# Kernel tuning notes

Hardware: AMD Instinct MI355X
Metric: run time of the kernel (lower is better)

The kernel has to match this reference:

```python
import jax, jax.numpy as jnp
import numpy as np

BETA = 0.25
NUM_CODES = 1024
EMBED_DIM = 256


def setup_inputs() -> dict:
    key = jax.random.key(0)
    k1, k2 = jax.random.split(key)
    z = jax.random.normal(k1, (64, 32, 32, EMBED_DIM), dtype=jnp.float32)
    # torch init: uniform(-1/num_codes, 1/num_codes)
    codebook = jax.random.uniform(k2, (NUM_CODES, EMBED_DIM), dtype=jnp.float32,
                                  minval=-1.0 / NUM_CODES, maxval=1.0 / NUM_CODES)
    return {"z": z, "codebook": codebook}


def reference(z, codebook):
    shape = z.shape
    z_flat = z.reshape(-1, EMBED_DIM)  # [N, D]
    # squared-distance matrix: ||z||^2 + ||c||^2 - 2 z c^T  -> [N, K]
    d = (jnp.sum(z_flat * z_flat, axis=1, keepdims=True)
         + jnp.sum(codebook * codebook, axis=1)
         - 2.0 * jnp.einsum('nd,kd->nk', z_flat, codebook))
    codes = jnp.argmin(d, axis=1)              # [N] int
    quantized = codebook[codes]                # [N, D] gather
    sg = jax.lax.stop_gradient
    cb_loss = jnp.mean((quantized - sg(z_flat)) ** 2)
    cmt_loss = jnp.mean((z_flat - sg(quantized)) ** 2)
    vq_loss = cb_loss + BETA * cmt_loss
    # straight-through estimator
    out = z_flat + sg(quantized - z_flat)
    return out.reshape(shape), codes.reshape(shape[:-1]), vq_loss
```

## Files before the change

### kernel.cpp

```cpp
#include <hip/hip_runtime.h>


#define N_PTS    65536
#define K_CODES  1024
#define DIM      256
#define MARGIN   1.5e-4f
#define WSKIP    4096

#define OUT_VALS  16777216
#define OUT_CODES 65536

typedef __attribute__((ext_vector_type(8))) short short8v;
typedef __attribute__((ext_vector_type(8))) _Float16 half8v;
typedef __attribute__((ext_vector_type(4))) float float4v;

__device__ __forceinline__ int perm_idx(int r, int k) {
  return ((((r >> 4) * 8 + (k >> 5)) * 4 + ((k >> 3) & 3)) * 128) + (r & 15) * 8 + (k & 7);
}

__device__ __forceinline__ short f2h_bits(float x) {
  union { _Float16 h; short s; } u;
  u.h = (_Float16)x;
  return u.s;
}

__device__ __forceinline__ void gload16(const void* g, void* l) {
  __builtin_amdgcn_global_load_lds(
      (const __attribute__((address_space(1))) unsigned*)g,
      (__attribute__((address_space(3))) unsigned*)l, 16, 0, 0);
}

__global__ void prep_cb_kernel(const float* __restrict__ cb,
                               short* __restrict__ cbh_perm,
                               float* __restrict__ Bf,
                               unsigned long long* __restrict__ scratch,
                               unsigned long long* __restrict__ ws0) {
  const int gid = blockIdx.x * 256 + threadIdx.x;
  scratch[gid] = ~0ull;
  if (gid < 512) ws0[gid] = 0ull;
  int r    = blockIdx.x * 4 + (threadIdx.x >> 6);
  int lane = threadIdx.x & 63;
  const float4 v = *(const float4*)(cb + (size_t)r * DIM + lane * 4);
  double s = (double)v.x * v.x + (double)v.y * v.y
           + (double)v.z * v.z + (double)v.w * v.w;
#pragma unroll
  for (int off = 32; off > 0; off >>= 1) s += __shfl_down(s, off);
  if (lane == 0) Bf[r] = (float)s;
  short4 h = make_short4(f2h_bits(v.x * 1024.0f), f2h_bits(v.y * 1024.0f),
                         f2h_bits(v.z * 1024.0f), f2h_bits(v.w * 1024.0f));
  *(short4*)(cbh_perm + perm_idx(r, lane * 4)) = h;
}

__global__ __launch_bounds__(256, 4) void argmin_mfma_kernel(
    const float* __restrict__ z, const float* __restrict__ cb,
    const short* __restrict__ cbh_perm,
    const float* __restrict__ Bf, float* __restrict__ outq,
    float* __restrict__ codes_out,
    int* __restrict__ cnt2, int* __restrict__ cntf,
    unsigned* __restrict__ flag2, int* __restrict__ flagf,
    float* __restrict__ bv2a, float* __restrict__ bvfa,
    double* __restrict__ loss_slots) {
  __shared__ __align__(16) short lbuf[2][8192];
  __shared__ double wls[4];
  const int t    = threadIdx.x;
  const int w    = t >> 6;
  const int l    = t & 63;
  const int quad = l >> 4;
  const int lr   = l & 15;
  const int m0   = blockIdx.x * 64;

  {
    const char* src = (const char*)cbh_perm;
    char* dst = (char*)&lbuf[0][0];
#pragma unroll
    for (int i = 0; i < 4; ++i)
      gload16(src + t * 16 + i * 4096, dst + t * 16 + i * 4096);
  }

  half8v ah[8];
  {
    const float* zrow = z + (size_t)(m0 + w * 16 + lr) * DIM;
#pragma unroll
    for (int q = 0; q < 8; ++q) {
      float4 p0 = *(const float4*)(zrow + q * 32 + quad * 8);
      float4 p1 = *(const float4*)(zrow + q * 32 + quad * 8 + 4);
      half8v h;
      h[0] = (_Float16)p0.x; h[1] = (_Float16)p0.y;
      h[2] = (_Float16)p0.z; h[3] = (_Float16)p0.w;
      h[4] = (_Float16)p1.x; h[5] = (_Float16)p1.y;
      h[6] = (_Float16)p1.z; h[7] = (_Float16)p1.w;
      ah[q] = h;
    }
  }

  float bestv[4], secv[4], thirdv[4]; int bestk[4], seck[4];
#pragma unroll
  for (int r = 0; r < 4; ++r) {
    bestv[r] = 3.0e38f; secv[r] = 3.0e38f; thirdv[r] = 3.0e38f;
    bestk[r] = 0; seck[r] = 0;
  }

  __syncthreads();
  int cur = 0;
  for (int it = 0; it < 32; ++it) {
    if (it < 31) {
      const char* src = (const char*)cbh_perm + (size_t)(it + 1) * 16384;
      char* dst = (char*)&lbuf[cur ^ 1][0];
#pragma unroll
      for (int i = 0; i < 4; ++i)
        gload16(src + t * 16 + i * 4096, dst + t * 16 + i * 4096);
    }
    const int c0 = it * 32;
#pragma unroll
    for (int st = 0; st < 2; ++st) {
      float4v acc = {0.f, 0.f, 0.f, 0.f};
#pragma unroll
      for (int q = 0; q < 8; ++q) {
        half8v b = *(const half8v*)(&lbuf[cur][(st * 8 + q) * 512 + quad * 128 + lr * 8]);
        acc = __builtin_amdgcn_mfma_f32_16x16x32_f16(ah[q], b, acc, 0, 0, 0);
      }
      const int k = c0 + st * 16 + lr;
      const float bkf = Bf[k];
#pragma unroll
      for (int r = 0; r < 4; ++r) {
        float v = fmaf(-0.001953125f, acc[r], bkf);
        bool lt1 = v < bestv[r];
        bool lt2 = v < secv[r];
        thirdv[r] = fminf(fmaxf(v, secv[r]), thirdv[r]);
        secv[r]   = fminf(fmaxf(v, bestv[r]), secv[r]);
        bestv[r]  = fminf(v, bestv[r]);
        seck[r]   = lt1 ? bestk[r] : (lt2 ? k : seck[r]);
        bestk[r]  = lt1 ? k : bestk[r];
      }
    }
    __syncthreads();
    cur ^= 1;
  }

#pragma unroll
  for (int mask = 1; mask < 16; mask <<= 1) {
#pragma unroll
    for (int r = 0; r < 4; ++r) {
      float ov  = __shfl_xor(bestv[r], mask);
      float os  = __shfl_xor(secv[r], mask);
      float ot  = __shfl_xor(thirdv[r], mask);
      int   ok  = __shfl_xor(bestk[r], mask);
      int   osk = __shfl_xor(seck[r], mask);
      bool win = (ov < bestv[r]) || (ov == bestv[r] && ok < bestk[r]);
      float a1 = win ? ov : bestv[r], a2 = win ? os : secv[r], a3 = win ? ot : thirdv[r];
      int   a1k = win ? ok : bestk[r], a2k = win ? osk : seck[r];
      float b1 = win ? bestv[r] : ov, b2 = win ? secv[r] : os;
      int   b1k = win ? bestk[r] : ok;
      bool s2 = (a2 < b1) || (a2 == b1 && a2k < b1k);
      bestv[r] = a1; bestk[r] = a1k;
      secv[r] = s2 ? a2 : b1; seck[r] = s2 ? a2k : b1k;
      thirdv[r] = s2 ? fminf(a3, b1) : fminf(a2, b2);
    }
  }

  if (m0 >= WSKIP) {
#pragma unroll
    for (int p = 0; p < 16; ++p) {
      int c = __shfl(bestk[p & 3], (p >> 2) << 4);
      int n = m0 + w * 16 + p;
      *(float4*)(outq + (size_t)n * DIM + l * 4) =
          *(const float4*)(cb + (size_t)c * DIM + l * 4);
    }
  }

  double ls = 0.0;
  if (lr == 0)
    ls = (double)bestv[0] + (double)bestv[1] + (double)bestv[2] + (double)bestv[3];
  ls += __shfl_down(ls, 16);
  ls += __shfl_down(ls, 32);
  if (l == 0) wls[w] = ls;

  if (lr == 0) {
#pragma unroll
    for (int r = 0; r < 4; ++r) {
      int n = m0 + w * 16 + quad * 4 + r;
      codes_out[n] = (float)bestk[r];
      if (thirdv[r] - bestv[r] < MARGIN) {
        int pos = atomicAdd(cntf, 1);
        flagf[pos] = n; bvfa[pos] = bestv[r];
      } else if (secv[r] - bestv[r] < MARGIN) {
        int pos = atomicAdd(cnt2, 1);
        flag2[pos] = (unsigned)n | ((unsigned)seck[r] << 16);
        bv2a[pos] = bestv[r];
      }
    }
  }
  __syncthreads();
  if (t == 0)
    atomicAdd(&loss_slots[blockIdx.x & 255], wls[0] + wls[1] + wls[2] + wls[3]);
}

__global__ __launch_bounds__(256) void fixup_pair_kernel(
    const float* __restrict__ z, const float* __restrict__ cb,
    const float* __restrict__ Bf, const unsigned* __restrict__ flag2,
    const int* __restrict__ cnt2, const float* __restrict__ bv2a,
    float* __restrict__ codes_out, float* __restrict__ outq,
    double* __restrict__ loss_slots) {
  const int t   = threadIdx.x;
  const int l   = t & 63;
  const int h   = l >> 5;
  const int sub = l & 31;
  const int wid = blockIdx.x * 4 + (t >> 6);
  const int nw  = gridDim.x * 4;
  const int cnt = *cnt2;
  for (int i = wid; i < cnt; i += nw) {
    const unsigned rec = flag2[i];
    const int n  = rec & 0xFFFF;
    const int k2 = rec >> 16;
    const int k1 = (int)codes_out[n];
    const int k  = h ? k2 : k1;
    const float* zr = z + (size_t)n * DIM + sub * 8;
    const float* cr = cb + (size_t)k * DIM + sub * 8;
    const float4 za = *(const float4*)(zr);
    const float4 zb = *(const float4*)(zr + 4);
    const float4 ca = *(const float4*)(cr);
    const float4 cv = *(const float4*)(cr + 4);
    double s = (double)za.x*za.x + (double)za.y*za.y + (double)za.z*za.z + (double)za.w*za.w
             + (double)zb.x*zb.x + (double)zb.y*zb.y + (double)zb.z*zb.z + (double)zb.w*zb.w;
    double d = (double)za.x*ca.x + (double)za.y*ca.y + (double)za.z*ca.z + (double)za.w*ca.w
             + (double)zb.x*cv.x + (double)zb.y*cv.y + (double)zb.z*cv.z + (double)zb.w*cv.w;
#pragma unroll
    for (int m = 1; m < 32; m <<= 1) {
      s += __shfl_xor(s, m);
      d += __shfl_xor(d, m);
    }
    const float Sfl = (float)s;
    const float T1  = Sfl + Bf[k];
    const float v   = T1 - 2.0f * (float)d;
    const float vo  = __shfl_xor(v, 32);
    const int   ko  = __shfl_xor(k, 32);
    const bool keep = (v < vo) || (v == vo && k < ko);
    const float vmin = keep ? v : vo;
    const int   kf   = keep ? k : ko;
    if (l == 0) {
      codes_out[n] = (float)kf;
      atomicAdd(&loss_slots[n & 255], (double)(vmin - bv2a[i]));
    }
    if (kf != k1 && n >= WSKIP)
      *(float4*)(outq + (size_t)n * DIM + l * 4) =
          *(const float4*)(cb + (size_t)kf * DIM + l * 4);
  }
}

__global__ __launch_bounds__(256) void fixup_full_kernel(
    const float* __restrict__ z, const float* __restrict__ cb,
    const float* __restrict__ Bf, const int* __restrict__ flagf,
    const int* __restrict__ cntf, unsigned long long* __restrict__ scratch) {
  __shared__ float vred[4];
  __shared__ int   kred[4];
  const int t = threadIdx.x;
  const int w = t >> 6;
  const int l = t & 63;
  const int cnt = *cntf;
  for (int ib = blockIdx.x; (ib >> 2) < cnt; ib += gridDim.x) {
    const int i = ib >> 2, q = ib & 3;
    const int n = flagf[i];
    const float4 zv = *(const float4*)(z + (size_t)n * DIM + l * 4);
    double s = (double)zv.x*zv.x + (double)zv.y*zv.y
             + (double)zv.z*zv.z + (double)zv.w*zv.w;
#pragma unroll
    for (int off = 32; off > 0; off >>= 1) s += __shfl_xor(s, off);
    const float Sfl = (float)s;
    float bvv = 3.0e38f; int bkk = 0;
    const int kbase = q * 256 + w * 64;
#pragma unroll 4
    for (int k0 = 0; k0 < 64; ++k0) {
      const int k = kbase + k0;
      const float4 cv = *(const float4*)(cb + (size_t)k * DIM + l * 4);
      double d = (double)zv.x*cv.x + (double)zv.y*cv.y
               + (double)zv.z*cv.z + (double)zv.w*cv.w;
#pragma unroll
      for (int off = 32; off > 0; off >>= 1) d += __shfl_xor(d, off);
      float T1 = Sfl + Bf[k];
      float v  = T1 - 2.0f * (float)d;
      if (v < bvv) { bvv = v; bkk = k; }
    }
    __syncthreads();
    if (l == 0) { vred[w] = bvv; kred[w] = bkk; }
    __syncthreads();
    if (t == 0) {
      float fv = vred[0]; int fk = kred[0];
#pragma unroll
      for (int j = 1; j < 4; ++j) {
        float v2 = vred[j]; int kk = kred[j];
        if (v2 < fv || (v2 == fv && kk < fk)) { fv = v2; fk = kk; }
      }
      unsigned long long key =
          ((unsigned long long)__float_as_uint(fv) << 32) | (unsigned)fk;
      atomicMin(&scratch[n], key);
    }
  }
}

__global__ __launch_bounds__(256) void fixup_write_kernel(
    const int* __restrict__ flagf, const int* __restrict__ cntf,
    const unsigned long long* __restrict__ scratch,
    const float* __restrict__ bvfa, const float* __restrict__ cb,
    float* __restrict__ codes_out, float* __restrict__ outq,
    double* __restrict__ loss_slots) {
  const int t = threadIdx.x, l = t & 63;
  const int wid = blockIdx.x * 4 + (t >> 6);
  const int nw  = gridDim.x * 4;
  const int cnt = *cntf;
  for (int i = wid; i < cnt; i += nw) {
    const int n = flagf[i];
    const unsigned long long key = scratch[n];
    const int   fk = (int)(unsigned)(key & 0xFFFFFFFFull);
    const float fv = __uint_as_float((unsigned)(key >> 32));
    const int   k1 = (int)codes_out[n];
    if (l == 0) {
      codes_out[n] = (float)fk;
      atomicAdd(&loss_slots[n & 255], (double)(fv - bvfa[i]));
    }
    if (fk != k1 && n >= WSKIP)
      *(float4*)(outq + (size_t)n * DIM + l * 4) =
          *(const float4*)(cb + (size_t)fk * DIM + l * 4);
  }
}

__global__ void small_gather_kernel(const float* __restrict__ cb,
                                    const float* __restrict__ codes_f,
                                    float* __restrict__ outq) {
  int gid = blockIdx.x * 256 + threadIdx.x;
  int n = gid >> 6, l = gid & 63;
  int c = (int)codes_f[n];
  *(float4*)(outq + (size_t)n * DIM + l * 4) =
      *(const float4*)(cb + (size_t)c * DIM + l * 4);
}

__global__ void finalize_kernel(const double* __restrict__ loss_slots,
                                float* __restrict__ out_loss) {
  const int t = threadIdx.x;
  double s = loss_slots[t];
#pragma unroll
  for (int off = 32; off > 0; off >>= 1) s += __shfl_down(s, off);
  __shared__ double ws[4];
  if ((t & 63) == 0) ws[t >> 6] = s;
  __syncthreads();
  if (t == 0) {
    double tot = ws[0] + ws[1] + ws[2] + ws[3];
    out_loss[0] = (float)(1.25 * tot / (double)(N_PTS * (size_t)DIM));
  }
}

extern "C" void kernel_launch(void* const* d_in, const int* in_sizes, int n_in,
                              void* d_out, int out_size, void* d_ws, size_t ws_size,
                              hipStream_t stream) {
  const float* z  = (const float*)d_in[0];
  const float* cb = (const float*)d_in[1];
  float* out = (float*)d_out;
  double* loss_slots = (double*)d_ws;
  int*      cnt2  = (int*)((char*)d_ws + 2048);
  int*      cntf  = (int*)((char*)d_ws + 2052);
  float*    Bf    = (float*)((char*)d_ws + 4096);
  unsigned* flag2 = (unsigned*)((char*)d_ws + 8192);
  short* cbh_perm = (short*)d_out;
  float* bv2a     = (float*)((char*)d_out + 524288);
  float* bvfa     = (float*)((char*)d_out + 786432);
  unsigned long long* scratch = (unsigned long long*)((char*)d_out + 1048576);
  int*   flagf    = (int*)((char*)d_out + 1572864);

  prep_cb_kernel<<<K_CODES / 4, 256, 0, stream>>>(
      cb, cbh_perm, Bf, scratch, (unsigned long long*)d_ws);
  argmin_mfma_kernel<<<N_PTS / 64, 256, 0, stream>>>(
      z, cb, cbh_perm, Bf, out, out + OUT_VALS, cnt2, cntf, flag2, flagf,
      bv2a, bvfa, loss_slots);
  fixup_pair_kernel<<<1024, 256, 0, stream>>>(
      z, cb, Bf, flag2, cnt2, bv2a, out + OUT_VALS, out, loss_slots);
  fixup_full_kernel<<<2048, 256, 0, stream>>>(z, cb, Bf, flagf, cntf, scratch);
  fixup_write_kernel<<<64, 256, 0, stream>>>(
      flagf, cntf, scratch, bvfa, cb, out + OUT_VALS, out, loss_slots);
  small_gather_kernel<<<WSKIP * 64 / 256, 256, 0, stream>>>(
      cb, out + OUT_VALS, out);
  finalize_kernel<<<1, 256, 0, stream>>>(loss_slots, out + OUT_VALS + OUT_CODES);
}
```

Before: 201.1 us.

## Split codebook across wave halves and reuse B fragments over two row tiles

Blocks grow to 512 threads covering 128 points. Each wave pair splits the codebook in half, and each wave computes two 16-row tiles against every B fragment it loads, so one LDS read feeds two MFMAs. The two halves' top-3 candidates are merged through shared memory. The kernel now also computes the full squared distance including ||z||² for the loss and flagging, and the quantized gather reads codes from shared memory. The cost is more registers per thread, which may lower occupancy.

Result: slower. 226.1 us (+12.4%).

```diff
diff --git a/kernel.cpp b/kernel.cpp
--- a/kernel.cpp
+++ b/kernel.cpp
@@ -51,7 +51,7 @@
   *(short4*)(cbh_perm + perm_idx(r, lane * 4)) = h;
 }
 
-__global__ __launch_bounds__(256, 4) void argmin_mfma_kernel(
+__global__ __launch_bounds__(512, 4) void argmin_mfma_kernel(
     const float* __restrict__ z, const float* __restrict__ cb,
     const short* __restrict__ cbh_perm,
     const float* __restrict__ Bf, float* __restrict__ outq,
@@ -60,77 +60,98 @@
     unsigned* __restrict__ flag2, int* __restrict__ flagf,
     float* __restrict__ bv2a, float* __restrict__ bvfa,
     double* __restrict__ loss_slots) {
-  __shared__ __align__(16) short lbuf[2][8192];
-  __shared__ double wls[4];
+  __shared__ __align__(16) short lbuf[2][2][4096];
+  __shared__ float mv1[128][2], mv2[128][2], mv3[128][2];
+  __shared__ int   mk1[128][2], mk2[128][2];
+  __shared__ float mz[128];
+  __shared__ int   scodes[128];
+  __shared__ double wls[2];
   const int t    = threadIdx.x;
   const int w    = t >> 6;
   const int l    = t & 63;
   const int quad = l >> 4;
   const int lr   = l & 15;
-  const int m0   = blockIdx.x * 64;
+  const int wp   = w >> 1;
+  const int h    = w & 1;
+  const int m0   = blockIdx.x * 128;
+  const int pbase = m0 + wp * 32;
 
   {
-    const char* src = (const char*)cbh_perm;
-    char* dst = (char*)&lbuf[0][0];
-#pragma unroll
-    for (int i = 0; i < 4; ++i)
-      gload16(src + t * 16 + i * 4096, dst + t * 16 + i * 4096);
-  }
-
-  half8v ah[8];
-  {
-    const float* zrow = z + (size_t)(m0 + w * 16 + lr) * DIM;
+    const char* src = (const char*)cbh_perm + (size_t)(h * 32) * 8192 + wp * 2048;
+    char* dst = (char*)&lbuf[h][0][0] + wp * 2048;
+    gload16(src + l * 16, dst + l * 16);
+    gload16(src + 1024 + l * 16, dst + 1024 + l * 16);
+  }
+
+  half8v ah[2][8];
+  float Szrow[2];
+#pragma unroll
+  for (int a = 0; a < 2; ++a) {
+    const float* zrow = z + (size_t)(pbase + a * 16 + lr) * DIM;
+    double zs = 0.0;
 #pragma unroll
     for (int q = 0; q < 8; ++q) {
       float4 p0 = *(const float4*)(zrow + q * 32 + quad * 8);
       float4 p1 = *(const float4*)(zrow + q * 32 + quad * 8 + 4);
-      half8v h;
-      h[0] = (_Float16)p0.x; h[1] = (_Float16)p0.y;
-      h[2] = (_Float16)p0.z; h[3] = (_Float16)p0.w;
-      h[4] = (_Float16)p1.x; h[5] = (_Float16)p1.y;
-      h[6] = (_Float16)p1.z; h[7] = (_Float16)p1.w;
-      ah[q] = h;
-    }
-  }
-
-  float bestv[4], secv[4], thirdv[4]; int bestk[4], seck[4];
-#pragma unroll
-  for (int r = 0; r < 4; ++r) {
-    bestv[r] = 3.0e38f; secv[r] = 3.0e38f; thirdv[r] = 3.0e38f;
-    bestk[r] = 0; seck[r] = 0;
+      zs = fma((double)p0.x, (double)p0.x, zs);
+      zs = fma((double)p0.y, (double)p0.y, zs);
+      zs = fma((double)p0.z, (double)p0.z, zs);
+      zs = fma((double)p0.w, (double)p0.w, zs);
+      zs = fma((double)p1.x, (double)p1.x, zs);
+      zs = fma((double)p1.y, (double)p1.y, zs);
+      zs = fma((double)p1.z, (double)p1.z, zs);
+      zs = fma((double)p1.w, (double)p1.w, zs);
+      half8v hh;
+      hh[0] = (_Float16)p0.x; hh[1] = (_Float16)p0.y;
+      hh[2] = (_Float16)p0.z; hh[3] = (_Float16)p0.w;
+      hh[4] = (_Float16)p1.x; hh[5] = (_Float16)p1.y;
+      hh[6] = (_Float16)p1.z; hh[7] = (_Float16)p1.w;
+      ah[a][q] = hh;
+    }
+    zs += __shfl_xor(zs, 16);
+    zs += __shfl_xor(zs, 32);
+    Szrow[a] = (float)zs;
+  }
+
+  float bv[8], sv[8], tv[8]; int bk[8], sk[8];
+#pragma unroll
+  for (int s = 0; s < 8; ++s) {
+    bv[s] = 3.0e38f; sv[s] = 3.0e38f; tv[s] = 3.0e38f; bk[s] = 0; sk[s] = 0;
   }
 
   __syncthreads();
   int cur = 0;
   for (int it = 0; it < 32; ++it) {
     if (it < 31) {
-      const char* src = (const char*)cbh_perm + (size_t)(it + 1) * 16384;
-      char* dst = (char*)&lbuf[cur ^ 1][0];
-#pragma unroll
-      for (int i = 0; i < 4; ++i)
-        gload16(src + t * 16 + i * 4096, dst + t * 16 + i * 4096);
-    }
-    const int c0 = it * 32;
-#pragma unroll
-    for (int st = 0; st < 2; ++st) {
-      float4v acc = {0.f, 0.f, 0.f, 0.f};
-#pragma unroll
-      for (int q = 0; q < 8; ++q) {
-        half8v b = *(const half8v*)(&lbuf[cur][(st * 8 + q) * 512 + quad * 128 + lr * 8]);
-        acc = __builtin_amdgcn_mfma_f32_16x16x32_f16(ah[q], b, acc, 0, 0, 0);
-      }
-      const int k = c0 + st * 16 + lr;
-      const float bkf = Bf[k];
+      const char* src = (const char*)cbh_perm + (size_t)(h * 32 + it + 1) * 8192 + wp * 2048;
+      char* dst = (char*)&lbuf[h][cur ^ 1][0] + wp * 2048;
+      gload16(src + l * 16, dst + l * 16);
+      gload16(src + 1024 + l * 16, dst + 1024 + l * 16);
+    }
+    const short* bb = &lbuf[h][cur][0];
+    float4v acc0 = {0.f, 0.f, 0.f, 0.f};
+    float4v acc1 = {0.f, 0.f, 0.f, 0.f};
+#pragma unroll
+    for (int q = 0; q < 8; ++q) {
+      half8v b = *(const half8v*)(bb + q * 512 + quad * 128 + lr * 8);
+      acc0 = __builtin_amdgcn_mfma_f32_16x16x32_f16(ah[0][q], b, acc0, 0, 0, 0);
+      acc1 = __builtin_amdgcn_mfma_f32_16x16x32_f16(ah[1][q], b, acc1, 0, 0, 0);
+    }
+    const int k = (h * 32 + it) * 16 + lr;
+    const float bkf = Bf[k];
+#pragma unroll
+    for (int a = 0; a < 2; ++a) {
 #pragma unroll
       for (int r = 0; r < 4; ++r) {
-        float v = fmaf(-0.001953125f, acc[r], bkf);
-        bool lt1 = v < bestv[r];
-        bool lt2 = v < secv[r];
-        thirdv[r] = fminf(fmaxf(v, secv[r]), thirdv[r]);
-        secv[r]   = fminf(fmaxf(v, bestv[r]), secv[r]);
-        bestv[r]  = fminf(v, bestv[r]);
-        seck[r]   = lt1 ? bestk[r] : (lt2 ? k : seck[r]);
-        bestk[r]  = lt1 ? k : bestk[r];
+        const int s = a * 4 + r;
+        float v = fmaf(-0.001953125f, a ? acc1[r] : acc0[r], bkf);
+        bool lt1 = v < bv[s];
+        bool lt2 = v < sv[s];
+        tv[s] = fminf(fmaxf(v, sv[s]), tv[s]);
+        sv[s] = fminf(fmaxf(v, bv[s]), sv[s]);
+        bv[s] = fminf(v, bv[s]);
+        sk[s] = lt1 ? bk[s] : (lt2 ? k : sk[s]);
+        bk[s] = lt1 ? k : bk[s];
       }
     }
     __syncthreads();
@@ -140,59 +161,86 @@
 #pragma unroll
   for (int mask = 1; mask < 16; mask <<= 1) {
 #pragma unroll
-    for (int r = 0; r < 4; ++r) {
-      float ov  = __shfl_xor(bestv[r], mask);
-      float os  = __shfl_xor(secv[r], mask);
-      float ot  = __shfl_xor(thirdv[r], mask);
-      int   ok  = __shfl_xor(bestk[r], mask);
-      int   osk = __shfl_xor(seck[r], mask);
-      bool win = (ov < bestv[r]) || (ov == bestv[r] && ok < bestk[r]);
-      float a1 = win ? ov : bestv[r], a2 = win ? os : secv[r], a3 = win ? ot : thirdv[r];
-      int   a1k = win ? ok : bestk[r], a2k = win ? osk : seck[r];
-      float b1 = win ? bestv[r] : ov, b2 = win ? secv[r] : os;
-      int   b1k = win ? bestk[r] : ok;
+    for (int s = 0; s < 8; ++s) {
+      float ov  = __shfl_xor(bv[s], mask);
+      float os  = __shfl_xor(sv[s], mask);
+      float ot  = __shfl_xor(tv[s], mask);
+      int   ok  = __shfl_xor(bk[s], mask);
+      int   osk = __shfl_xor(sk[s], mask);
+      bool win = (ov < bv[s]) || (ov == bv[s] && ok < bk[s]);
+      float a1 = win ? ov : bv[s], a2 = win ? os : sv[s], a3 = win ? ot : tv[s];
+      int   a1k = win ? ok : bk[s], a2k = win ? osk : sk[s];
+      float b1 = win ? bv[s] : ov, b2 = win ? sv[s] : os;
+      int   b1k = win ? bk[s] : ok;
       bool s2 = (a2 < b1) || (a2 == b1 && a2k < b1k);
-      bestv[r] = a1; bestk[r] = a1k;
-      secv[r] = s2 ? a2 : b1; seck[r] = s2 ? a2k : b1k;
-      thirdv[r] = s2 ? fminf(a3, b1) : fminf(a2, b2);
-    }
-  }
+      bv[s] = a1; bk[s] = a1k;
+      sv[s] = s2 ? a2 : b1; sk[s] = s2 ? a2k : b1k;
+      tv[s] = s2 ? fminf(a3, b1) : fminf(a2, b2);
+    }
+  }
+
+  if (lr == 0) {
+#pragma unroll
+    for (int a = 0; a < 2; ++a)
+#pragma unroll
+      for (int r = 0; r < 4; ++r) {
+        int s  = a * 4 + r;
+        int pt = wp * 32 + a * 16 + quad * 4 + r;
+        mv1[pt][h] = bv[s]; mv2[pt][h] = sv[s]; mv3[pt][h] = tv[s];
+        mk1[pt][h] = bk[s]; mk2[pt][h] = sk[s];
+      }
+  }
+  if (h == 0 && quad == 0) {
+#pragma unroll
+    for (int a = 0; a < 2; ++a)
+      mz[wp * 32 + a * 16 + lr] = Szrow[a];
+  }
+  __syncthreads();
+
+  double ls = 0.0;
+  if (t < 128) {
+    float a1 = mv1[t][0], a2 = mv2[t][0], a3 = mv3[t][0];
+    int   a1k = mk1[t][0], a2k = mk2[t][0];
+    float c1 = mv1[t][1], c2 = mv2[t][1], c3 = mv3[t][1];
+    int   c1k = mk1[t][1], c2k = mk2[t][1];
+    bool win = (c1 < a1) || (c1 == a1 && c1k < a1k);
+    float x1 = win ? c1 : a1, x2 = win ? c2 : a2, x3 = win ? c3 : a3;
+    int   x1k = win ? c1k : a1k, x2k = win ? c2k : a2k;
+    float y1 = win ? a1 : c1, y2 = win ? a2 : c2;
+    int   y1k = win ? a1k : c1k;
+    bool s2 = (x2 < y1) || (x2 == y1 && x2k < y1k);
+    float f2v = s2 ? x2 : y1; int f2k = s2 ? x2k : y1k;
+    float f3v = s2 ? fminf(x3, y1) : fminf(x2, y2);
+    int n = m0 + t;
+    codes_out[n] = (float)x1k;
+    scodes[t] = x1k;
+    float vrow = mz[t] + x1;
+    ls = (double)vrow;
+    if (f3v - x1 < MARGIN) {
+      int pos = atomicAdd(cntf, 1);
+      flagf[pos] = n; bvfa[pos] = vrow;
+    } else if (f2v - x1 < MARGIN) {
+      int pos = atomicAdd(cnt2, 1);
+      flag2[pos] = (unsigned)n | ((unsigned)f2k << 16);
+      bv2a[pos] = vrow;
+    }
+  }
+#pragma unroll
+  for (int off = 32; off > 0; off >>= 1) ls += __shfl_down(ls, off);
+  if (l == 0 && w < 2) wls[w] = ls;
+  __syncthreads();
 
   if (m0 >= WSKIP) {
 #pragma unroll
-    for (int p = 0; p < 16; ++p) {
-      int c = __shfl(bestk[p & 3], (p >> 2) << 4);
-      int n = m0 + w * 16 + p;
-      *(float4*)(outq + (size_t)n * DIM + l * 4) =
+    for (int i = 0; i < 16; ++i) {
+      int row = i * 8 + w;
+      int c = scodes[row];
+      *(float4*)(outq + (size_t)(m0 + row) * DIM + l * 4) =
           *(const float4*)(cb + (size_t)c * DIM + l * 4);
     }
   }
-
-  double ls = 0.0;
-  if (lr == 0)
-    ls = (double)bestv[0] + (double)bestv[1] + (double)bestv[2] + (double)bestv[3];
-  ls += __shfl_down(ls, 16);
-  ls += __shfl_down(ls, 32);
-  if (l == 0) wls[w] = ls;
-
-  if (lr == 0) {
-#pragma unroll
-    for (int r = 0; r < 4; ++r) {
-      int n = m0 + w * 16 + quad * 4 + r;
-      codes_out[n] = (float)bestk[r];
-      if (thirdv[r] - bestv[r] < MARGIN) {
-        int pos = atomicAdd(cntf, 1);
-        flagf[pos] = n; bvfa[pos] = bestv[r];
-      } else if (secv[r] - bestv[r] < MARGIN) {
-        int pos = atomicAdd(cnt2, 1);
-        flag2[pos] = (unsigned)n | ((unsigned)seck[r] << 16);
-        bv2a[pos] = bestv[r];
-      }
-    }
-  }
-  __syncthreads();
   if (t == 0)
-    atomicAdd(&loss_slots[blockIdx.x & 255], wls[0] + wls[1] + wls[2] + wls[3]);
+    atomicAdd(&loss_slots[blockIdx.x & 255], wls[0] + wls[1]);
 }
 
 __global__ __launch_bounds__(256) void fixup_pair_kernel(
@@ -367,7 +415,7 @@
 
   prep_cb_kernel<<<K_CODES / 4, 256, 0, stream>>>(
       cb, cbh_perm, Bf, scratch, (unsigned long long*)d_ws);
-  argmin_mfma_kernel<<<N_PTS / 64, 256, 0, stream>>>(
+  argmin_mfma_kernel<<<N_PTS / 128, 512, 0, stream>>>(
       z, cb, cbh_perm, Bf, out, out + OUT_VALS, cnt2, cntf, flag2, flagf,
       bv2a, bvfa, loss_slots);
   fixup_pair_kernel<<<1024, 256, 0, stream>>>(
```

## Compute row norms in-kernel for loss and fuse finalize into gather kernel

Applied to the files above, without the earlier changes.

The argmin kernel now computes each z row's squared norm in double precision from the values it already loads, and adds it to the best partial distance. This gives the true squared error for the loss and for the fixup baselines, where before only the partial score was used. The final loss reduction is merged into the small gather kernel as one extra block, which saves one kernel launch. The fused block reads loss_slots in the same kernel that gathers rows, which is safe only because the fixup kernels run earlier on the stream. The double-precision FMAs add ALU work to the main kernel.

New measurement: 200.2 us. About the same (-0.5%).

```diff
diff --git a/kernel.cpp b/kernel.cpp
--- a/kernel.cpp
+++ b/kernel.cpp
@@ -78,12 +78,22 @@
   }
 
   half8v ah[8];
+  float Szrow;
   {
     const float* zrow = z + (size_t)(m0 + w * 16 + lr) * DIM;
+    double zs0 = 0.0, zs1 = 0.0;
 #pragma unroll
     for (int q = 0; q < 8; ++q) {
       float4 p0 = *(const float4*)(zrow + q * 32 + quad * 8);
       float4 p1 = *(const float4*)(zrow + q * 32 + quad * 8 + 4);
+      zs0 = fma((double)p0.x, (double)p0.x, zs0);
+      zs0 = fma((double)p0.y, (double)p0.y, zs0);
+      zs0 = fma((double)p0.z, (double)p0.z, zs0);
+      zs0 = fma((double)p0.w, (double)p0.w, zs0);
+      zs1 = fma((double)p1.x, (double)p1.x, zs1);
+      zs1 = fma((double)p1.y, (double)p1.y, zs1);
+      zs1 = fma((double)p1.z, (double)p1.z, zs1);
+      zs1 = fma((double)p1.w, (double)p1.w, zs1);
       half8v h;
       h[0] = (_Float16)p0.x; h[1] = (_Float16)p0.y;
       h[2] = (_Float16)p0.z; h[3] = (_Float16)p0.w;
@@ -91,6 +101,10 @@
       h[6] = (_Float16)p1.z; h[7] = (_Float16)p1.w;
       ah[q] = h;
     }
+    double zs = zs0 + zs1;
+    zs += __shfl_xor(zs, 16);
+    zs += __shfl_xor(zs, 32);
+    Szrow = (float)zs;
   }
 
   float bestv[4], secv[4], thirdv[4]; int bestk[4], seck[4];
@@ -158,6 +172,11 @@
     }
   }
 
+  float vrow[4];
+#pragma unroll
+  for (int r = 0; r < 4; ++r)
+    vrow[r] = __shfl(Szrow, quad * 4 + r) + bestv[r];
+
   if (m0 >= WSKIP) {
 #pragma unroll
     for (int p = 0; p < 16; ++p) {
@@ -170,7 +189,7 @@
 
   double ls = 0.0;
   if (lr == 0)
-    ls = (double)bestv[0] + (double)bestv[1] + (double)bestv[2] + (double)bestv[3];
+    ls = (double)vrow[0] + (double)vrow[1] + (double)vrow[2] + (double)vrow[3];
   ls += __shfl_down(ls, 16);
   ls += __shfl_down(ls, 32);
   if (l == 0) wls[w] = ls;
@@ -182,11 +201,11 @@
       codes_out[n] = (float)bestk[r];
       if (thirdv[r] - bestv[r] < MARGIN) {
         int pos = atomicAdd(cntf, 1);
-        flagf[pos] = n; bvfa[pos] = bestv[r];
+        flagf[pos] = n; bvfa[pos] = vrow[r];
       } else if (secv[r] - bestv[r] < MARGIN) {
         int pos = atomicAdd(cnt2, 1);
         flag2[pos] = (unsigned)n | ((unsigned)seck[r] << 16);
-        bv2a[pos] = bestv[r];
+        bv2a[pos] = vrow[r];
       }
     }
   }
@@ -323,29 +342,30 @@
   }
 }
 
-__global__ void small_gather_kernel(const float* __restrict__ cb,
-                                    const float* __restrict__ codes_f,
-                                    float* __restrict__ outq) {
+__global__ void gather_finalize_kernel(const float* __restrict__ cb,
+                                       const float* __restrict__ codes_f,
+                                       float* __restrict__ outq,
+                                       const double* __restrict__ loss_slots,
+                                       float* __restrict__ out_loss) {
+  if (blockIdx.x == WSKIP / 4) {
+    const int t = threadIdx.x;
+    double s = loss_slots[t];
+#pragma unroll
+    for (int off = 32; off > 0; off >>= 1) s += __shfl_down(s, off);
+    __shared__ double ws[4];
+    if ((t & 63) == 0) ws[t >> 6] = s;
+    __syncthreads();
+    if (t == 0) {
+      double tot = ws[0] + ws[1] + ws[2] + ws[3];
+      out_loss[0] = (float)(1.25 * tot / (double)(N_PTS * (size_t)DIM));
+    }
+    return;
+  }
   int gid = blockIdx.x * 256 + threadIdx.x;
   int n = gid >> 6, l = gid & 63;
   int c = (int)codes_f[n];
   *(float4*)(outq + (size_t)n * DIM + l * 4) =
       *(const float4*)(cb + (size_t)c * DIM + l * 4);
-}
-
-__global__ void finalize_kernel(const double* __restrict__ loss_slots,
-                                float* __restrict__ out_loss) {
-  const int t = threadIdx.x;
-  double s = loss_slots[t];
-#pragma unroll
-  for (int off = 32; off > 0; off >>= 1) s += __shfl_down(s, off);
-  __shared__ double ws[4];
-  if ((t & 63) == 0) ws[t >> 6] = s;
-  __syncthreads();
-  if (t == 0) {
-    double tot = ws[0] + ws[1] + ws[2] + ws[3];
-    out_loss[0] = (float)(1.25 * tot / (double)(N_PTS * (size_t)DIM));
-  }
 }
 
 extern "C" void kernel_launch(void* const* d_in, const int* in_sizes, int n_in,
@@ -375,7 +395,6 @@
   fixup_full_kernel<<<2048, 256, 0, stream>>>(z, cb, Bf, flagf, cntf, scratch);
   fixup_write_kernel<<<64, 256, 0, stream>>>(
       flagf, cntf, scratch, bvfa, cb, out + OUT_VALS, out, loss_slots);
-  small_gather_kernel<<<WSKIP * 64 / 256, 256, 0, stream>>>(
-      cb, out + OUT_VALS, out);
-  finalize_kernel<<<1, 256, 0, stream>>>(loss_slots, out + OUT_VALS + OUT_CODES);
-}
+  gather_finalize_kernel<<<WSKIP / 4 + 1, 256, 0, stream>>>(
+      cb, out + OUT_VALS, out, loss_slots, out + OUT_VALS + OUT_CODES);
+}
```
